# Performance work log

Hardware: AMD Instinct MI355X
Metric: run time of the kernel (lower is better)

## Reference

```python
import jax, jax.numpy as jnp
import numpy as np

# --- static anchor geometry (exactly mirrors RPN._make_anchor_box) ---

def _valid_idx():
    scales = [64.0, 128.0, 256.0]
    ratios = [0.5, 1.0, 2.0]
    # (h, w) per anchor, normalized by 448
    anc = np.array([[s / np.sqrt(r), s * np.sqrt(r)] for s in scales for r in ratios]) / 448.0
    c = (np.arange(28) + 0.5) / 28.0
    cy = np.repeat(c, 28).reshape(28, 28)  # y varies along rows
    cx = np.tile(c, (28, 1))               # x varies along cols
    boxes = np.zeros((28, 28, 36))
    for a in range(9):
        boxes[..., 4 * a + 0] = cy
        boxes[..., 4 * a + 1] = cx
        boxes[..., 4 * a + 2] = anc[a, 0]
        boxes[..., 4 * a + 3] = anc[a, 1]
    b = boxes.reshape(-1, 4)  # [7056, 4] in yxhw
    y1 = b[:, 0] - b[:, 2] / 2
    x1 = b[:, 1] - b[:, 3] / 2
    y2 = b[:, 0] + b[:, 2] / 2
    x2 = b[:, 1] + b[:, 3] / 2
    return np.where((y1 > 0) & (x1 > 0) & (y2 < 28) & (x2 < 28))[0]

_VALID = _valid_idx()  # 4850 static indices

ROI_CLS_THRESHOLD = 0.9


def setup_inputs() -> dict:
    key = jax.random.key(0)
    ks = jax.random.split(key, 4)
    C = 2048
    return {
        'x': jax.random.normal(ks[0], (1, C, 28, 28), jnp.float32),
        'conv_w': jax.random.normal(ks[1], (C, C, 3, 3), jnp.float32) * 0.02,
        'conv_b': jnp.zeros((C,), jnp.float32),
        'reg_w': jax.random.normal(ks[2], (36, C), jnp.float32) * 0.02,
        'reg_b': jnp.zeros((36,), jnp.float32),
        'cls_w': jax.random.normal(ks[3], (9, C), jnp.float32) * 0.02,
        'cls_b': jnp.zeros((9,), jnp.float32),
    }


def reference(x, conv_w, conv_b, reg_w, reg_b, cls_w, cls_b):
    # Conv block: 3x3 conv + BatchNorm(identity at init: gamma=1, beta=0, running stats 0/1) + ReLU
    h = jax.lax.conv_general_dilated(
        x, conv_w, window_strides=(1, 1), padding=((1, 1), (1, 1)),
        dimension_numbers=('NCHW', 'OIHW', 'NCHW'))
    h = jax.nn.relu(h + conv_b[None, :, None, None])
    # 1x1 conv heads + sigmoid
    reg = jax.nn.sigmoid(jnp.einsum('bchw,oc->bohw', h, reg_w) + reg_b[None, :, None, None])  # [1,36,28,28]
    cls = jax.nn.sigmoid(jnp.einsum('bchw,oc->bohw', h, cls_w) + cls_b[None, :, None, None])  # [1,9,28,28]
    # exact replication of view/permute/squeeze + static valid-anchor gather
    reg = reg.reshape(1, 4, -1).transpose(0, 2, 1)[0][_VALID]  # [4850, 4]
    cls = cls.reshape(-1)[_VALID]                              # [4850]
    # inference path (gt=None): reg[cls > 0.9]; fixed-shape masked equivalent
    keep = cls > ROI_CLS_THRESHOLD
    return reg * keep[:, None]
```

## Files before the change

### kernel.cpp

```cpp
#include <hip/hip_runtime.h>
#include <cstdint>

typedef __attribute__((ext_vector_type(8))) short s8v;
typedef __attribute__((ext_vector_type(4))) float f4v;

__device__ __forceinline__ unsigned short bf16_rne(float f) {
    unsigned u = __float_as_uint(f);
    u += 0x7FFFu + ((u >> 16) & 1u);
    return (unsigned short)(u >> 16);
}
__device__ __forceinline__ float bf16f(unsigned short h) {
    return __uint_as_float(((unsigned)h) << 16);
}
__device__ __forceinline__ void cvt2(float a, float b, unsigned& hiw, unsigned& low) {
    unsigned ua = __float_as_uint(a), ub = __float_as_uint(b);
    unsigned ha = ua + 0x7FFFu + ((ua >> 16) & 1u);
    unsigned hb = ub + 0x7FFFu + ((ub >> 16) & 1u);
    hiw = (ha >> 16) | (hb & 0xFFFF0000u);
    float ra = a - __uint_as_float(ha & 0xFFFF0000u);
    float rb = b - __uint_as_float(hb & 0xFFFF0000u);
    unsigned la = __float_as_uint(ra), lb = __float_as_uint(rb);
    la += 0x7FFFu + ((la >> 16) & 1u);
    lb += 0x7FFFu + ((lb >> 16) & 1u);
    low = (la >> 16) | (lb & 0xFFFF0000u);
}
__device__ __forceinline__ void cvt2t(float a, float b, unsigned& hiw, unsigned& low) {
    unsigned ua = __float_as_uint(a), ub = __float_as_uint(b);
    hiw = (ua >> 16) | (ub & 0xFFFF0000u);
    float ra = a - __uint_as_float(ua & 0xFFFF0000u);
    float rb = b - __uint_as_float(ub & 0xFFFF0000u);
    unsigned la = __float_as_uint(ra), lb = __float_as_uint(rb);
    low = (la >> 16) | (lb & 0xFFFF0000u);
}

__global__ __launch_bounds__(256) void transpose_x(const float* __restrict__ x,
                                                   float* __restrict__ xt) {
    __shared__ float t[64][65];
    int c0 = blockIdx.x * 64, p0 = blockIdx.y * 64;
    int l = threadIdx.x & 63, g = threadIdx.x >> 6;
#pragma unroll
    for (int j = 0; j < 16; ++j) {
        int cc = j * 4 + g;
        int p = p0 + l;
        t[cc][l] = (p < 784) ? x[(size_t)(c0 + cc) * 784 + p] : 0.f;
    }
    __syncthreads();
#pragma unroll
    for (int j = 0; j < 16; ++j) {
        int pp = j * 4 + g;
        int p = p0 + pp;
        if (p < 784) xt[(size_t)p * 2048 + c0 + l] = t[l][pp];
    }
}

__global__ __launch_bounds__(256) void build_B(const float* __restrict__ xt,
                                               unsigned* __restrict__ Bhi,
                                               unsigned* __restrict__ Blo) {
    int p = blockIdx.x;
    int h = p / 28, w = p % 28;
#pragma unroll
    for (int it = 0; it < 4; ++it) {
        int cp = it * 256 + threadIdx.x;
        float va[18];
#pragma unroll
        for (int r = 0; r < 9; ++r) {
            int h2 = h + r / 3 - 1, w2 = w + r % 3 - 1;
            bool ok = (h2 >= 0) & (h2 < 28) & (w2 >= 0) & (w2 < 28);
            float2 v = ok ? ((const float2*)(xt + (size_t)(h2 * 28 + w2) * 2048))[cp]
                          : float2{0.f, 0.f};
            va[r] = v.x;
            va[9 + r] = v.y;
        }
        size_t base = (size_t)p * 9216 + (size_t)cp * 9;
#pragma unroll
        for (int d = 0; d < 9; ++d) {
            unsigned hw, lw;
            cvt2(va[2 * d], va[2 * d + 1], hw, lw);
            Bhi[base + d] = hw;
            Blo[base + d] = lw;
        }
    }
}

#define AHI_OFF 0
#define ALO_OFF 8192
#define BHI_OFF 16384
#define BLO_OFF 23552
#define LDS_BYTES 30720
#define KCH 1152
#define NSTEP 36

__global__ __launch_bounds__(256, 4) void conv_gemm(const float* __restrict__ cw,
                                                    const char* __restrict__ wsb,
                                                    uint32_t offBhi, uint32_t offBlo,
                                                    float* __restrict__ part) {
    __shared__ char smem[LDS_BYTES];
    int tid = threadIdx.x;
    int lane = tid & 63, wave = tid >> 6;
    int bm0 = blockIdx.x * 128, bn0 = blockIdx.y * 112, z = blockIdx.z;

    uint32_t doff[4], dlds[4];
#pragma unroll
    for (int j = 0; j < 4; ++j) {
        int i = j * 4 + wave;
        if (i >= 14) i -= 2;
        bool hiP = i < 7;
        int jj = hiP ? i : i - 7;
        int prow = jj * 16 + (lane >> 2);
        int pos = lane & 3;
        int gblk = pos ^ ((prow >> 1) & 3);
        uint32_t elem = (uint32_t)(bn0 + prow) * 18432 + (uint32_t)z * KCH + gblk * 8;
        doff[j] = (hiP ? offBhi : offBlo) + elem * 2;
        dlds[j] = (hiP ? BHI_OFF : BLO_OFF) + jj * 1024;
    }

    int m = lane & 15, qd = lane >> 4;
    int sw = (m >> 1) & 3;
    uint32_t apos = (uint32_t)(wave * 32 + m) * 64 + (uint32_t)((qd ^ sw) * 16);
    uint32_t bpos = (uint32_t)m * 64 + (uint32_t)((qd ^ sw) * 16);
    int arow = tid >> 1, ahalf = tid & 1;
    int swt = (arow >> 1) & 3;

    f4v acc[2][7];
#pragma unroll
    for (int a = 0; a < 2; ++a)
#pragma unroll
        for (int b = 0; b < 7; ++b) acc[a][b] = f4v{0.f, 0.f, 0.f, 0.f};

    const float4* ap = (const float4*)(cw + (size_t)(bm0 + arow) * 18432 + (size_t)z * KCH
                                       + (size_t)ahalf * 16);
    float4 arc[4], arn[4];
#pragma unroll
    for (int j = 0; j < 4; ++j) arc[j] = ap[j];

    for (int step = 0; step < NSTEP; ++step) {
#pragma unroll
        for (int j = 0; j < 4; ++j) {
            __builtin_amdgcn_global_load_lds(
                (const __attribute__((address_space(1))) void*)(wsb + doff[j]),
                (__attribute__((address_space(3))) void*)(smem + dlds[j]), 16, 0, 0);
            doff[j] += 64;
        }
        if (step < NSTEP - 1) {
            ap += 8;
#pragma unroll
            for (int j = 0; j < 4; ++j) arn[j] = ap[j];
        }
        unsigned hw[8], lw[8];
#pragma unroll
        for (int j = 0; j < 4; ++j) {
            cvt2t(arc[j].x, arc[j].y, hw[2 * j], lw[2 * j]);
            cvt2t(arc[j].z, arc[j].w, hw[2 * j + 1], lw[2 * j + 1]);
        }
#pragma unroll
        for (int b = 0; b < 2; ++b) {
            uint32_t col = (uint32_t)(((2 * ahalf + b) ^ swt) * 16);
            *(uint4*)(smem + AHI_OFF + arow * 64 + col) =
                uint4{hw[4 * b], hw[4 * b + 1], hw[4 * b + 2], hw[4 * b + 3]};
            *(uint4*)(smem + ALO_OFF + arow * 64 + col) =
                uint4{lw[4 * b], lw[4 * b + 1], lw[4 * b + 2], lw[4 * b + 3]};
        }
        __syncthreads();

        s8v ah[2], al[2];
#pragma unroll
        for (int mt = 0; mt < 2; ++mt) {
            ah[mt] = *(const s8v*)(smem + AHI_OFF + apos + mt * 1024);
            al[mt] = *(const s8v*)(smem + ALO_OFF + apos + mt * 1024);
        }
#pragma unroll
        for (int nt = 0; nt < 7; ++nt) {
            s8v bh = *(const s8v*)(smem + BHI_OFF + bpos + nt * 1024);
            s8v bl = *(const s8v*)(smem + BLO_OFF + bpos + nt * 1024);
#pragma unroll
            for (int mt = 0; mt < 2; ++mt) {
                acc[mt][nt] = __builtin_amdgcn_mfma_f32_16x16x32_bf16(ah[mt], bh, acc[mt][nt], 0, 0, 0);
                acc[mt][nt] = __builtin_amdgcn_mfma_f32_16x16x32_bf16(ah[mt], bl, acc[mt][nt], 0, 0, 0);
                acc[mt][nt] = __builtin_amdgcn_mfma_f32_16x16x32_bf16(al[mt], bh, acc[mt][nt], 0, 0, 0);
            }
        }
        __syncthreads();

        if (step < NSTEP - 1) {
#pragma unroll
            for (int j = 0; j < 4; ++j) arc[j] = arn[j];
        }
    }

    float* pz = part + (size_t)z * 1605632;
#pragma unroll
    for (int mt = 0; mt < 2; ++mt) {
        int o = bm0 + wave * 32 + mt * 16 + qd * 4;
#pragma unroll
        for (int nt = 0; nt < 7; ++nt) {
            int p = bn0 + nt * 16 + m;
            *(float4*)(pz + (size_t)p * 2048 + o) =
                float4{acc[mt][nt].x, acc[mt][nt].y, acc[mt][nt].z, acc[mt][nt].w};
        }
    }
}

__constant__ int HMIN_d[9] = {3, 2, 1, 6, 4, 3, 11, 8, 6};
__constant__ int WMIN_d[9] = {1, 2, 3, 3, 4, 6, 6, 8, 11};

__global__ __launch_bounds__(256) void heads(const float* __restrict__ part,
                                             const float* __restrict__ conv_b,
                                             const float* __restrict__ reg_w,
                                             const float* __restrict__ reg_b,
                                             const float* __restrict__ cls_w,
                                             const float* __restrict__ cls_b,
                                             float* __restrict__ out) {
    int tid = threadIdx.x;
    int lane = tid & 63, wave = tid >> 6;
    int p = blockIdx.x;
    int ci = tid * 2;

    float4 h0 = ((const float4*)conv_b)[ci];
    float4 h1 = ((const float4*)conv_b)[ci + 1];
#pragma unroll
    for (int z = 0; z < 16; ++z) {
        const float4* pz = (const float4*)(part + (size_t)z * 1605632 + (size_t)p * 2048);
        float4 a = pz[ci], b = pz[ci + 1];
        h0.x += a.x; h0.y += a.y; h0.z += a.z; h0.w += a.w;
        h1.x += b.x; h1.y += b.y; h1.z += b.z; h1.w += b.w;
    }
    h0.x = fmaxf(h0.x, 0.f); h0.y = fmaxf(h0.y, 0.f);
    h0.z = fmaxf(h0.z, 0.f); h0.w = fmaxf(h0.w, 0.f);
    h1.x = fmaxf(h1.x, 0.f); h1.y = fmaxf(h1.y, 0.f);
    h1.z = fmaxf(h1.z, 0.f); h1.w = fmaxf(h1.w, 0.f);

    float s[45];
#pragma unroll
    for (int o = 0; o < 36; ++o) {
        float4 wa = ((const float4*)(reg_w + (size_t)o * 2048))[ci];
        float4 wb = ((const float4*)(reg_w + (size_t)o * 2048))[ci + 1];
        s[o] = h0.x * wa.x + h0.y * wa.y + h0.z * wa.z + h0.w * wa.w +
               h1.x * wb.x + h1.y * wb.y + h1.z * wb.z + h1.w * wb.w;
    }
#pragma unroll
    for (int a = 0; a < 9; ++a) {
        float4 wa = ((const float4*)(cls_w + (size_t)a * 2048))[ci];
        float4 wb = ((const float4*)(cls_w + (size_t)a * 2048))[ci + 1];
        s[36 + a] = h0.x * wa.x + h0.y * wa.y + h0.z * wa.z + h0.w * wa.w +
                    h1.x * wb.x + h1.y * wb.y + h1.z * wb.z + h1.w * wb.w;
    }

    __shared__ float wsum[4][45];
    __shared__ float fin[45];
#pragma unroll
    for (int o = 0; o < 45; ++o) {
        float v = s[o];
#pragma unroll
        for (int d = 1; d < 64; d <<= 1) v += __shfl_xor(v, d, 64);
        if (lane == 0) wsum[wave][o] = v;
    }
    __syncthreads();
    if (tid < 45) fin[tid] = wsum[0][tid] + wsum[1][tid] + wsum[2][tid] + wsum[3][tid];
    __syncthreads();

    if (tid < 9) {
        int ap = tid;
        int n = ap * 784 + p;
        int pix = n / 9, a2 = n % 9;
        int hh = pix / 28, ww = pix % 28;
        if (hh >= HMIN_d[a2] && ww >= WMIN_d[a2]) {
            int row = 0;
#pragma unroll
            for (int a3 = 0; a3 < 9; ++a3) {
                int hm = HMIN_d[a3], wm = WMIN_d[a3];
                int full = hh - hm; if (full < 0) full = 0;
                row += full * (28 - wm);
                if (hh >= hm) { int prt = ww - wm; if (prt < 0) prt = 0; row += prt; }
                if (a3 < a2 && hh >= hm && ww >= wm) row += 1;
            }
            float cl = fin[36 + ap] + cls_b[ap];
            float keep = (1.f / (1.f + expf(-cl)) > 0.9f) ? 1.f : 0.f;
#pragma unroll
            for (int q = 0; q < 4; ++q) {
                float rl = fin[q * 9 + ap] + reg_b[q * 9 + ap];
                out[row * 4 + q] = keep / (1.f + expf(-rl));
            }
        }
    }
}

extern "C" void kernel_launch(void* const* d_in, const int* in_sizes, int n_in,
                              void* d_out, int out_size, void* d_ws, size_t ws_size,
                              hipStream_t stream) {
    const float* x = (const float*)d_in[0];
    const float* conv_w = (const float*)d_in[1];
    const float* conv_b = (const float*)d_in[2];
    const float* reg_w = (const float*)d_in[3];
    const float* reg_b = (const float*)d_in[4];
    const float* cls_w = (const float*)d_in[5];
    const float* cls_b = (const float*)d_in[6];
    float* out = (float*)d_out;
    char* ws = (char*)d_ws;

    const size_t o_part = 0;
    const size_t o_xt = 0;
    const size_t o_Bhi = 102760448;
    const size_t o_Blo = 131661824;

    transpose_x<<<dim3(32, 13), 256, 0, stream>>>(x, (float*)(ws + o_xt));
    build_B<<<784, 256, 0, stream>>>((const float*)(ws + o_xt), (unsigned*)(ws + o_Bhi),
                                     (unsigned*)(ws + o_Blo));
    conv_gemm<<<dim3(16, 7, 16), 256, 0, stream>>>(conv_w, ws, (uint32_t)o_Bhi,
                                                   (uint32_t)o_Blo, (float*)(ws + o_part));
    heads<<<784, 256, 0, stream>>>((const float*)(ws + o_part), conv_b, reg_w, reg_b,
                                   cls_w, cls_b, out);
}
```

Measured before the change: 488.7 us.

## Double-buffer LDS tiles in conv GEMM to overlap loads with MFMA

Converts the conv GEMM main loop to double-buffered shared memory. The next step's B tile (async global->LDS) and converted A tile are written into the alternate buffer while MFMAs consume the current one, which removes one __syncthreads per step. It also raises wave priority around the MFMA block. LDS use doubles to 60KB and launch bounds drop from 4 to 2 blocks per CU, so occupancy falls in exchange for the overlap.

Measured after the change: 524.0 us. +7.2%, slower.

```diff
diff --git a/kernel.cpp b/kernel.cpp
--- a/kernel.cpp
+++ b/kernel.cpp
@@ -82,15 +82,11 @@
     }
 }
 
-#define AHI_OFF 0
-#define ALO_OFF 8192
-#define BHI_OFF 16384
-#define BLO_OFF 23552
-#define LDS_BYTES 30720
 #define KCH 1152
 #define NSTEP 36
-
-__global__ __launch_bounds__(256, 4) void conv_gemm(const float* __restrict__ cw,
+#define LDS_BYTES 61440
+
+__global__ __launch_bounds__(256, 2) void conv_gemm(const float* __restrict__ cw,
                                                     const char* __restrict__ wsb,
                                                     uint32_t offBhi, uint32_t offBlo,
                                                     float* __restrict__ part) {
@@ -99,7 +95,7 @@
     int lane = tid & 63, wave = tid >> 6;
     int bm0 = blockIdx.x * 128, bn0 = blockIdx.y * 112, z = blockIdx.z;
 
-    uint32_t doff[4], dlds[4];
+    uint32_t doff[4], dldsB[4];
 #pragma unroll
     for (int j = 0; j < 4; ++j) {
         int i = j * 4 + wave;
@@ -111,7 +107,7 @@
         int gblk = pos ^ ((prow >> 1) & 3);
         uint32_t elem = (uint32_t)(bn0 + prow) * 18432 + (uint32_t)z * KCH + gblk * 8;
         doff[j] = (hiP ? offBhi : offBlo) + elem * 2;
-        dlds[j] = (hiP ? BHI_OFF : BLO_OFF) + jj * 1024;
+        dldsB[j] = (hiP ? 0u : 7168u) + (uint32_t)jj * 1024;
     }
 
     int m = lane & 15, qd = lane >> 4;
@@ -129,49 +125,74 @@
 
     const float4* ap = (const float4*)(cw + (size_t)(bm0 + arow) * 18432 + (size_t)z * KCH
                                        + (size_t)ahalf * 16);
-    float4 arc[4], arn[4];
-#pragma unroll
-    for (int j = 0; j < 4; ++j) arc[j] = ap[j];
-
-    for (int step = 0; step < NSTEP; ++step) {
+    float4 ar[4];
+#pragma unroll
+    for (int j = 0; j < 4; ++j) ar[j] = ap[j];
+
+    auto writeA = [&](char* smA) {
+        unsigned hw[8], lw[8];
 #pragma unroll
         for (int j = 0; j < 4; ++j) {
-            __builtin_amdgcn_global_load_lds(
-                (const __attribute__((address_space(1))) void*)(wsb + doff[j]),
-                (__attribute__((address_space(3))) void*)(smem + dlds[j]), 16, 0, 0);
-            doff[j] += 64;
-        }
-        if (step < NSTEP - 1) {
-            ap += 8;
-#pragma unroll
-            for (int j = 0; j < 4; ++j) arn[j] = ap[j];
-        }
-        unsigned hw[8], lw[8];
-#pragma unroll
-        for (int j = 0; j < 4; ++j) {
-            cvt2t(arc[j].x, arc[j].y, hw[2 * j], lw[2 * j]);
-            cvt2t(arc[j].z, arc[j].w, hw[2 * j + 1], lw[2 * j + 1]);
+            cvt2t(ar[j].x, ar[j].y, hw[2 * j], lw[2 * j]);
+            cvt2t(ar[j].z, ar[j].w, hw[2 * j + 1], lw[2 * j + 1]);
         }
 #pragma unroll
         for (int b = 0; b < 2; ++b) {
             uint32_t col = (uint32_t)(((2 * ahalf + b) ^ swt) * 16);
-            *(uint4*)(smem + AHI_OFF + arow * 64 + col) =
+            *(uint4*)(smA + arow * 64 + col) =
                 uint4{hw[4 * b], hw[4 * b + 1], hw[4 * b + 2], hw[4 * b + 3]};
-            *(uint4*)(smem + ALO_OFF + arow * 64 + col) =
+            *(uint4*)(smA + 8192 + arow * 64 + col) =
                 uint4{lw[4 * b], lw[4 * b + 1], lw[4 * b + 2], lw[4 * b + 3]};
         }
-        __syncthreads();
+    };
+
+#pragma unroll
+    for (int j = 0; j < 4; ++j) {
+        __builtin_amdgcn_global_load_lds(
+            (const __attribute__((address_space(1))) void*)(wsb + doff[j]),
+            (__attribute__((address_space(3))) void*)(smem + 32768 + dldsB[j]), 16, 0, 0);
+        doff[j] += 64;
+    }
+    writeA(smem);
+    ap += 8;
+#pragma unroll
+    for (int j = 0; j < 4; ++j) ar[j] = ap[j];
+    __syncthreads();
+
+#pragma unroll 2
+    for (int step = 0; step < NSTEP; ++step) {
+        int buf = step & 1, nbuf = buf ^ 1;
+        char* smA = smem + buf * 16384;
+        char* smB = smem + 32768 + buf * 14336;
+
+        if (step < NSTEP - 1) {
+            char* smBn = smem + 32768 + nbuf * 14336;
+#pragma unroll
+            for (int j = 0; j < 4; ++j) {
+                __builtin_amdgcn_global_load_lds(
+                    (const __attribute__((address_space(1))) void*)(wsb + doff[j]),
+                    (__attribute__((address_space(3))) void*)(smBn + dldsB[j]), 16, 0, 0);
+                doff[j] += 64;
+            }
+            writeA(smem + nbuf * 16384);
+            if (step < NSTEP - 2) {
+                ap += 8;
+#pragma unroll
+                for (int j = 0; j < 4; ++j) ar[j] = ap[j];
+            }
+        }
 
         s8v ah[2], al[2];
 #pragma unroll
         for (int mt = 0; mt < 2; ++mt) {
-            ah[mt] = *(const s8v*)(smem + AHI_OFF + apos + mt * 1024);
-            al[mt] = *(const s8v*)(smem + ALO_OFF + apos + mt * 1024);
-        }
+            ah[mt] = *(const s8v*)(smA + apos + mt * 1024);
+            al[mt] = *(const s8v*)(smA + 8192 + apos + mt * 1024);
+        }
+        __builtin_amdgcn_s_setprio(1);
 #pragma unroll
         for (int nt = 0; nt < 7; ++nt) {
-            s8v bh = *(const s8v*)(smem + BHI_OFF + bpos + nt * 1024);
-            s8v bl = *(const s8v*)(smem + BLO_OFF + bpos + nt * 1024);
+            s8v bh = *(const s8v*)(smB + bpos + nt * 1024);
+            s8v bl = *(const s8v*)(smB + 7168 + bpos + nt * 1024);
 #pragma unroll
             for (int mt = 0; mt < 2; ++mt) {
                 acc[mt][nt] = __builtin_amdgcn_mfma_f32_16x16x32_bf16(ah[mt], bh, acc[mt][nt], 0, 0, 0);
@@ -179,12 +200,8 @@
                 acc[mt][nt] = __builtin_amdgcn_mfma_f32_16x16x32_bf16(al[mt], bh, acc[mt][nt], 0, 0, 0);
             }
         }
+        __builtin_amdgcn_s_setprio(0);
         __syncthreads();
-
-        if (step < NSTEP - 1) {
-#pragma unroll
-            for (int j = 0; j < 4; ++j) arc[j] = arn[j];
-        }
     }
 
     float* pz = part + (size_t)z * 1605632;
```
